# Optimization experiments

Hardware: AMD Instinct MI355X
Metric: run time of the kernel (lower is better)

Reference implementation:

```python
import jax, jax.numpy as jnp
import numpy as np

# Static config matching init_kwargs / forward constants
H = 12          # num_heads
D = 64          # head_dim
SW = 64         # kv_cache_sliding_window (frames)
SF = 8          # kv_cache_scale_frames
NUM_REG = 4     # num_register_tokens -> camera_idx=0, scale_idx=5
SPECIAL_END = NUM_REG + 2  # camera..scale inclusive slice = tokens [0:6)


def setup_inputs() -> dict:
    key = jax.random.key(0)
    ks = jax.random.split(key, 9)
    B, N, C = 1, 576, 768
    T = 192  # tokens per frame; num_frame_per_block = N // T = 3
    inp = {
        'x': jax.random.normal(ks[0], (B, N, C), jnp.float32),
        'qkv_w': jax.random.normal(ks[1], (3 * C, C), jnp.float32) * (C ** -0.5),
        'qkv_b': jax.random.normal(ks[2], (3 * C,), jnp.float32) * 0.02,
        'proj_w': jax.random.normal(ks[3], (C, C), jnp.float32) * (C ** -0.5),
        'proj_b': jax.random.normal(ks[4], (C,), jnp.float32) * 0.02,
        'k_cache': jax.random.normal(ks[5], (B, H, SW + SF, T, D), jnp.float32),
        'v_cache': jax.random.normal(ks[6], (B, H, SW + SF, T, D), jnp.float32),
        'k_special': jax.random.normal(ks[7], (B, H, 12, SPECIAL_END, D), jnp.float32),
        'v_special': jax.random.normal(ks[8], (B, H, 12, SPECIAL_END, D), jnp.float32),
    }
    return inp


def reference(x, qkv_w, qkv_b, proj_w, proj_b, k_cache, v_cache, k_special, v_special):
    B, N, C = x.shape
    T = k_cache.shape[3]           # tokens per frame
    nfb = N // T                   # num_frame_per_block (inferred, as in torch code)

    # qkv projection: (B,N,3C) -> (3,B,H,N,D)
    qkv = (x @ qkv_w.T + qkv_b).reshape(B, N, 3, H, D).transpose(2, 0, 3, 1, 4)
    q, k, v = qkv[0], qkv[1], qkv[2]   # each (B,H,N,D); q_norm/k_norm = Identity

    # Append new block frames to the cache
    k_cache = jnp.concatenate([k_cache, k.reshape(B, H, nfb, T, D)], axis=2)
    v_cache = jnp.concatenate([v_cache, v.reshape(B, H, nfb, T, D)], axis=2)

    # Sliding-window eviction (shapes chosen so this branch always fires)
    F = k_cache.shape[2]
    evict_start, evict_end = SF, F - SW   # 8 .. 11
    # cross-frame special tokens: camera..scale (tokens 0:6) of evicted frames
    new_sk = k_cache[:, :, evict_start:evict_end, :SPECIAL_END, :]
    new_sv = v_cache[:, :, evict_start:evict_end, :SPECIAL_END, :]
    k_special = jnp.concatenate([k_special, new_sk], axis=2)
    v_special = jnp.concatenate([v_special, new_sv], axis=2)
    # keep scale frames + last sliding_window frames
    k_cache = jnp.concatenate([k_cache[:, :, :SF], k_cache[:, :, -SW:]], axis=2)
    v_cache = jnp.concatenate([v_cache[:, :, :SF], v_cache[:, :, -SW:]], axis=2)

    # Flatten frames -> tokens; prepend special tokens
    k_full = jnp.concatenate([k_special.reshape(B, H, -1, D),
                              k_cache.reshape(B, H, -1, D)], axis=2)
    v_full = jnp.concatenate([v_special.reshape(B, H, -1, D),
                              v_cache.reshape(B, H, -1, D)], axis=2)

    # SDPA (no mask, no dropout, default scale 1/sqrt(D))
    scale = 1.0 / jnp.sqrt(jnp.float32(D))
    scores = jnp.einsum('bhnd,bhmd->bhnm', q, k_full) * scale
    attn = jax.nn.softmax(scores, axis=-1)
    out = jnp.einsum('bhnm,bhmd->bhnd', attn, v_full)

    out = out.transpose(0, 2, 1, 3).reshape(B, N, H * D)
    return out @ proj_w.T + proj_b
```

## Files before the change

### kernel.cpp

```cpp
#include <hip/hip_runtime.h>
#include <hip/hip_bf16.h>

#define NH    12
#define HD    64
#define NT    576
#define CC    768
#define M_TOT 13914
#define MP    13952
#define NTIL  218
#define NEW0  13338
#define SSTR  16

typedef short bf16x8 __attribute__((ext_vector_type(8)));
typedef float f32x4 __attribute__((ext_vector_type(4)));
typedef float f32x16 __attribute__((ext_vector_type(16)));

__device__ __forceinline__ unsigned pk2(float a, float b) {
  __hip_bfloat162 h = __float22bfloat162_rn(make_float2(a, b));
  return *(unsigned*)&h;
}

__global__ __launch_bounds__(256) void cvt_all(
    const float* __restrict__ x, const float* __restrict__ wsrc,
    __hip_bfloat16* __restrict__ xb, __hip_bfloat16* __restrict__ wb) {
  const int nx8 = NT * CC / 8;
  const int nw8 = 3 * CC * CC / 8;
  int i = blockIdx.x * 256 + threadIdx.x;
  const float* src;
  __hip_bfloat16* dst;
  int j;
  if (i < nx8) { src = x; dst = xb; j = i; }
  else { j = i - nx8; if (j >= nw8) return; src = wsrc; dst = wb; }
  const float4 a = ((const float4*)src)[2 * j];
  const float4 b = ((const float4*)src)[2 * j + 1];
  __hip_bfloat16 t[8];
  t[0] = __float2bfloat16(a.x); t[1] = __float2bfloat16(a.y);
  t[2] = __float2bfloat16(a.z); t[3] = __float2bfloat16(a.w);
  t[4] = __float2bfloat16(b.x); t[5] = __float2bfloat16(b.y);
  t[6] = __float2bfloat16(b.z); t[7] = __float2bfloat16(b.w);
  ((uint4*)dst)[j] = *(const uint4*)t;
}

__device__ __forceinline__ const float* kv_src_row(
    const float* __restrict__ cache, const float* __restrict__ special,
    int h, int m) {
  if (m < 72) return special + ((size_t)h * 72 + m) * HD;
  if (m < 90) {
    const int j = m - 72;
    return cache + (((size_t)h * 72 + 8 + j / 6) * 192 + (j % 6)) * HD;
  }
  if (m < 1626) return cache + ((size_t)h * 13824 + (m - 90)) * HD;
  return cache + ((size_t)h * 13824 + 2112 + (m - 1626)) * HD;
}

#define GEMM_BLKS 324
#define VT_BLKS   2616
#define KB_BLKS   10004

__global__ __launch_bounds__(256) void qkv_and_gather(
    const __hip_bfloat16* __restrict__ xb, const __hip_bfloat16* __restrict__ wb,
    const float* __restrict__ bias, __hip_bfloat16* __restrict__ Qb,
    __hip_bfloat16* __restrict__ Kf, __hip_bfloat16* __restrict__ Vt,
    const float* __restrict__ kc, const float* __restrict__ ksp,
    const float* __restrict__ vc, const float* __restrict__ vsp) {
  __shared__ float vsf[64][68];
  const int bx = blockIdx.x;
  const int tid = threadIdx.x;

  if (bx < GEMM_BLKS) {
    const int w = tid >> 6, l = tid & 63, l15 = l & 15, lg = l >> 4;
    const int n0 = (bx % 36) * 64;
    const int mw = (bx / 36) * 64 + w * 16;

    f32x4 acc[4];
#pragma unroll
    for (int nt = 0; nt < 4; ++nt) acc[nt] = (f32x4){0.f, 0.f, 0.f, 0.f};

    const __hip_bfloat16* arow = xb + (size_t)(mw + l15) * CC + 8 * lg;
#pragma unroll 4
    for (int k0 = 0; k0 < CC; k0 += 32) {
      const bf16x8 a = *(const bf16x8*)(arow + k0);
#pragma unroll
      for (int nt = 0; nt < 4; ++nt) {
        const bf16x8 b =
            *(const bf16x8*)(wb + (size_t)(n0 + nt * 16 + l15) * CC + k0 + 8 * lg);
        acc[nt] = __builtin_amdgcn_mfma_f32_16x16x32_bf16(a, b, acc[nt], 0, 0, 0);
      }
    }
#pragma unroll
    for (int nt = 0; nt < 4; ++nt) {
      const int c = n0 + nt * 16 + l15;
      const int which = c / CC;
      const int rem = c - which * CC;
      const int hh = rem >> 6;
      const int dd = rem & 63;
      const float bc = bias[c];
#pragma unroll
      for (int r = 0; r < 4; ++r) {
        const int m = mw + 4 * lg + r;
        const float v = acc[nt][r] + bc;
        if (which == 0) {
          Qb[((size_t)hh * NT + m) * HD + dd] = __float2bfloat16(v * 0.125f);
        } else if (which == 1) {
          Kf[((size_t)hh * MP + NEW0 + m) * HD + dd] = __float2bfloat16(v);
        } else {
          Vt[((size_t)hh * HD + dd) * MP + NEW0 + m] = __float2bfloat16(v);
        }
      }
    }
  } else if (bx < GEMM_BLKS + VT_BLKS) {
    const int tv = bx - GEMM_BLKS;
    const int m0 = (tv % 218) * 64;
    const int h = tv / 218;
    if (m0 >= NEW0) return;
#pragma unroll
    for (int p = 0; p < 4; ++p) {
      const int mr = m0 + p * 16 + (tid >> 4);
      const int c4 = (tid & 15) * 4;
      float4 v = make_float4(0.f, 0.f, 0.f, 0.f);
      if (mr < NEW0) v = *(const float4*)(kv_src_row(vc, vsp, h, mr) + c4);
      *(float4*)&vsf[p * 16 + (tid >> 4)][c4] = v;
    }
    __syncthreads();
#pragma unroll
    for (int e0 = 0; e0 < 2; ++e0) {
      const int e = tid + e0 * 256;
      const int d = e >> 3;
      const int ms = (e & 7) * 8;
      __hip_bfloat16 t[8];
#pragma unroll
      for (int j = 0; j < 8; ++j) t[j] = __float2bfloat16(vsf[ms + j][d]);
      __hip_bfloat16* dst = Vt + ((size_t)h * HD + d) * MP + m0 + ms;
      if (m0 + ms + 8 <= NEW0) {
        *(uint4*)dst = *(const uint4*)t;
      } else {
#pragma unroll
        for (int j = 0; j < 8; ++j)
          if (m0 + ms + j < NEW0) dst[j] = t[j];
      }
    }
  } else {
    const int idx = (bx - GEMM_BLKS - VT_BLKS) * 256 + tid;
    const int per_h = NEW0 * 16;
    if (idx >= NH * per_h) return;
    const int h = idx / per_h;
    const int r = idx - h * per_h;
    const int m = r >> 4;
    const int dq = (r & 15) << 2;
    const float4 v = *(const float4*)(kv_src_row(kc, ksp, h, m) + dq);
    __hip_bfloat162* dst = (__hip_bfloat162*)(Kf + ((size_t)h * MP + m) * HD + dq);
    __hip_bfloat162 a, b;
    a.x = __float2bfloat16(v.x); a.y = __float2bfloat16(v.y);
    b.x = __float2bfloat16(v.z); b.y = __float2bfloat16(v.w);
    dst[0] = a; dst[1] = b;
  }
}

__global__ __launch_bounds__(256, 4) void attn_partial(
    const __hip_bfloat16* __restrict__ Qb, const __hip_bfloat16* __restrict__ Kf,
    const __hip_bfloat16* __restrict__ Vt, float* __restrict__ Opart,
    float2* __restrict__ mlpart) {
  __shared__ __align__(16) char lds[16384];
  char* ksb = lds;
  char* vtb = lds + 8192;

  const int tid = threadIdx.x;
  const int w = tid >> 6, l = tid & 63;
  const int l31 = l & 31, hi = l >> 5;

  const int i = blockIdx.x;
  const int work = (i & 7) * 120 + (i >> 3);
  const int qt = work % 5;
  const int hs = work / 5;
  const int h = hs % NH;
  const int strip = hs / NH;

  const int qrow = qt * 128 + w * 32 + l31;
  const int qrc = qrow < NT ? qrow : NT - 1;

  bf16x8 qreg[4];
  {
    const __hip_bfloat16* qp = Qb + ((size_t)h * NT + qrc) * HD + 8 * hi;
#pragma unroll
    for (int s4 = 0; s4 < 4; ++s4) qreg[s4] = *(const bf16x8*)(qp + 16 * s4);
  }

  f32x16 oacc0, oacc1;
#pragma unroll
  for (int r = 0; r < 16; ++r) { oacc0[r] = 0.f; oacc1[r] = 0.f; }
  float m_run = -1e30f, l_run = 0.f;

  const __hip_bfloat16* Kh = Kf + (size_t)h * MP * HD;
  const __hip_bfloat16* Vth = Vt + (size_t)h * HD * MP;

  for (int t = strip; t < NTIL; t += SSTR) {
    const int m0 = t * 64;
#pragma unroll
    for (int e = 0; e < 2; ++e) {
      const int c = tid + 256 * e;
      const int row = c >> 3, p = c & 7;
      const unsigned off = ((unsigned)((row << 7) | (p << 4))) ^ ((row & 7) << 4);
      const uint4 kd = *(const uint4*)(Kh + (size_t)(m0 + row) * HD + p * 8);
      const uint4 vd = *(const uint4*)(Vth + (size_t)row * MP + m0 + p * 8);
      *(uint4*)(ksb + off) = kd;
      *(uint4*)(vtb + off) = vd;
    }
    __syncthreads();

    f32x16 sc0, sc1;
#pragma unroll
    for (int r = 0; r < 16; ++r) { sc0[r] = 0.f; sc1[r] = 0.f; }
#pragma unroll
    for (int s4 = 0; s4 < 4; ++s4) {
      const int cb = 32 * s4 + 16 * hi;
      const unsigned o0 = ((unsigned)((l31 << 7) | cb)) ^ ((l31 & 7) << 4);
      const unsigned o1 = ((unsigned)(((l31 + 32) << 7) | cb)) ^ ((l31 & 7) << 4);
      const bf16x8 a0 = *(const bf16x8*)(ksb + o0);
      const bf16x8 a1 = *(const bf16x8*)(ksb + o1);
      sc0 = __builtin_amdgcn_mfma_f32_32x32x16_bf16(a0, qreg[s4], sc0, 0, 0, 0);
      sc1 = __builtin_amdgcn_mfma_f32_32x32x16_bf16(a1, qreg[s4], sc1, 0, 0, 0);
    }

    if (m0 + 64 > M_TOT) {
#pragma unroll
      for (int r = 0; r < 16; ++r) {
        const int base = (r & 3) + 8 * (r >> 2) + 4 * hi;
        if (m0 + base >= M_TOT) sc0[r] = -1e30f;
        if (m0 + 32 + base >= M_TOT) sc1[r] = -1e30f;
      }
    }

    float mt = sc0[0];
#pragma unroll
    for (int r = 1; r < 16; ++r) mt = fmaxf(mt, sc0[r]);
#pragma unroll
    for (int r = 0; r < 16; ++r) mt = fmaxf(mt, sc1[r]);
    mt = fmaxf(mt, __shfl_xor(mt, 32));

    if (__any(mt > m_run + 8.f)) {
      const float mn = fmaxf(m_run, mt);
      const float corr = __expf(m_run - mn);
      m_run = mn;
      l_run *= corr;
#pragma unroll
      for (int r = 0; r < 16; ++r) { oacc0[r] *= corr; oacc1[r] *= corr; }
    }

    float psum = 0.f;
    unsigned W0[8], W1[8];
#pragma unroll
    for (int i2 = 0; i2 < 8; ++i2) {
      const float e0 = __expf(sc0[2 * i2] - m_run);
      const float e1 = __expf(sc0[2 * i2 + 1] - m_run);
      const float f0 = __expf(sc1[2 * i2] - m_run);
      const float f1 = __expf(sc1[2 * i2 + 1] - m_run);
      psum += (e0 + e1) + (f0 + f1);
      W0[i2] = pk2(e0, e1);
      W1[i2] = pk2(f0, f1);
    }
    psum += __shfl_xor(psum, 32);
    l_run += psum;

#pragma unroll
    for (int s4 = 0; s4 < 4; ++s4) {
      const int u = s4 & 1;
      const unsigned a0 = (s4 < 2) ? W0[4 * u + 0] : W1[4 * u + 0];
      const unsigned a1 = (s4 < 2) ? W0[4 * u + 1] : W1[4 * u + 1];
      const unsigned a2 = (s4 < 2) ? W0[4 * u + 2] : W1[4 * u + 2];
      const unsigned a3 = (s4 < 2) ? W0[4 * u + 3] : W1[4 * u + 3];
      const unsigned x0 = (unsigned)__shfl_xor((int)a0, 32);
      const unsigned x1 = (unsigned)__shfl_xor((int)a1, 32);
      const unsigned x2 = (unsigned)__shfl_xor((int)a2, 32);
      const unsigned x3 = (unsigned)__shfl_xor((int)a3, 32);
      union { unsigned u4[4]; bf16x8 v; } pa;
      pa.u4[0] = hi ? x2 : a0;
      pa.u4[1] = hi ? x3 : a1;
      pa.u4[2] = hi ? a2 : x0;
      pa.u4[3] = hi ? a3 : x1;
      const int cb = 32 * s4 + 16 * hi;
#pragma unroll
      for (int dh = 0; dh < 2; ++dh) {
        const int vr = 32 * dh + l31;
        const unsigned ov = ((unsigned)((vr << 7) | cb)) ^ ((vr & 7) << 4);
        const bf16x8 va = *(const bf16x8*)(vtb + ov);
        if (dh == 0)
          oacc0 = __builtin_amdgcn_mfma_f32_32x32x16_bf16(va, pa.v, oacc0, 0, 0, 0);
        else
          oacc1 = __builtin_amdgcn_mfma_f32_32x32x16_bf16(va, pa.v, oacc1, 0, 0, 0);
      }
    }
    __syncthreads();
  }

  if (qrow < NT) {
    float* Op = Opart + (((size_t)strip * NH + h) * NT + qrow) * HD;
#pragma unroll
    for (int g = 0; g < 4; ++g) {
      f32x4 o0 = {oacc0[4 * g], oacc0[4 * g + 1], oacc0[4 * g + 2], oacc0[4 * g + 3]};
      f32x4 o1 = {oacc1[4 * g], oacc1[4 * g + 1], oacc1[4 * g + 2], oacc1[4 * g + 3]};
      *(f32x4*)(Op + 8 * g + 4 * hi) = o0;
      *(f32x4*)(Op + 32 + 8 * g + 4 * hi) = o1;
    }
    if (hi == 0)
      mlpart[((size_t)strip * NH + h) * NT + qrow] = make_float2(m_run, l_run);
  }
}

__global__ __launch_bounds__(256) void attn_merge(
    const float* __restrict__ Opart, const float2* __restrict__ mlpart,
    float* __restrict__ Ow) {
  const int idx = blockIdx.x * 256 + threadIdx.x;
  if (idx >= NH * NT * HD) return;
  const int d = idx & 63;
  const int hn = idx >> 6;
  const int n = hn % NT;
  const int h = hn / NT;
  float M = -1e30f;
  float m[SSTR], lv[SSTR];
#pragma unroll
  for (int s = 0; s < SSTR; ++s) {
    const float2 ml = mlpart[((size_t)s * NH + h) * NT + n];
    m[s] = ml.x; lv[s] = ml.y;
    M = fmaxf(M, m[s]);
  }
  float L = 0.f, O = 0.f;
#pragma unroll
  for (int s = 0; s < SSTR; ++s) {
    const float e = __expf(m[s] - M);
    L += lv[s] * e;
    O += Opart[(((size_t)s * NH + h) * NT + n) * HD + d] * e;
  }
  Ow[(size_t)n * CC + h * HD + d] = O / L;
}

__global__ __launch_bounds__(256) void gemm_proj(
    const float* __restrict__ A, const float* __restrict__ W,
    const float* __restrict__ bias, float* __restrict__ out_f) {
  __shared__ float xs[32][36];
  __shared__ float wsT[32][68];
  const int tid = threadIdx.x;
  const int tx = tid & 15, ty = tid >> 4;
  const int bm = blockIdx.y * 32, bn = blockIdx.x * 64;
  float acc[2][4] = {{0.f, 0.f, 0.f, 0.f}, {0.f, 0.f, 0.f, 0.f}};
  for (int k0 = 0; k0 < CC; k0 += 32) {
    {
      const int r = tid >> 3, kq = (tid & 7) << 2;
      *(float4*)&xs[r][kq] = *(const float4*)(A + (size_t)(bm + r) * CC + k0 + kq);
    }
#pragma unroll
    for (int e0 = 0; e0 < 2; ++e0) {
      const int e = tid + e0 * 256;
      const int r = e >> 3, kq = (e & 7) << 2;
      float4 v = *(const float4*)(W + (size_t)(bn + r) * CC + k0 + kq);
      wsT[kq + 0][r] = v.x; wsT[kq + 1][r] = v.y;
      wsT[kq + 2][r] = v.z; wsT[kq + 3][r] = v.w;
    }
    __syncthreads();
#pragma unroll
    for (int kk = 0; kk < 32; ++kk) {
      const float a0 = xs[ty * 2 + 0][kk];
      const float a1 = xs[ty * 2 + 1][kk];
      const float4 b = *(const float4*)&wsT[kk][tx * 4];
      acc[0][0] = fmaf(a0, b.x, acc[0][0]); acc[0][1] = fmaf(a0, b.y, acc[0][1]);
      acc[0][2] = fmaf(a0, b.z, acc[0][2]); acc[0][3] = fmaf(a0, b.w, acc[0][3]);
      acc[1][0] = fmaf(a1, b.x, acc[1][0]); acc[1][1] = fmaf(a1, b.y, acc[1][1]);
      acc[1][2] = fmaf(a1, b.z, acc[1][2]); acc[1][3] = fmaf(a1, b.w, acc[1][3]);
    }
    __syncthreads();
  }
#pragma unroll
  for (int i = 0; i < 2; ++i)
#pragma unroll
    for (int j = 0; j < 4; ++j) {
      const int m = bm + ty * 2 + i, c = bn + tx * 4 + j;
      out_f[(size_t)m * CC + c] = acc[i][j] + bias[c];
    }
}

extern "C" void kernel_launch(void* const* d_in, const int* in_sizes, int n_in,
                              void* d_out, int out_size, void* d_ws,
                              size_t ws_size, hipStream_t stream) {
  const float* x       = (const float*)d_in[0];
  const float* qkv_w   = (const float*)d_in[1];
  const float* qkv_b   = (const float*)d_in[2];
  const float* proj_w  = (const float*)d_in[3];
  const float* proj_b  = (const float*)d_in[4];
  const float* k_cache = (const float*)d_in[5];
  const float* v_cache = (const float*)d_in[6];
  const float* k_specl = (const float*)d_in[7];
  const float* v_specl = (const float*)d_in[8];
  float* out = (float*)d_out;

  const size_t qb_bytes = (size_t)NH * NT * HD * 2;
  const size_t kv_bytes = (size_t)NH * MP * HD * 2;
  const size_t xb_bytes = (size_t)NT * CC * 2;
  const size_t op_bytes = (size_t)SSTR * NH * NT * HD * 4;
  const size_t ml_bytes = (size_t)SSTR * NH * NT * 8;

  char* ws = (char*)d_ws;
  __hip_bfloat16* Qb = (__hip_bfloat16*)ws;
  __hip_bfloat16* Kf = (__hip_bfloat16*)(ws + qb_bytes);
  __hip_bfloat16* Vt = (__hip_bfloat16*)(ws + qb_bytes + kv_bytes);
  char* opp = ws + qb_bytes + 2 * kv_bytes;
  float* Opart = (float*)opp;
  __hip_bfloat16* xb = (__hip_bfloat16*)opp;
  __hip_bfloat16* wb = (__hip_bfloat16*)(opp + xb_bytes);
  float2* mlpart = (float2*)(opp + op_bytes);
  float* Ow = (float*)(opp + op_bytes + ml_bytes);

  cvt_all<<<dim3(1080), 256, 0, stream>>>(x, qkv_w, xb, wb);
  qkv_and_gather<<<dim3(GEMM_BLKS + VT_BLKS + KB_BLKS), 256, 0, stream>>>(
      xb, wb, qkv_b, Qb, Kf, Vt, k_cache, k_specl, v_cache, v_specl);
  attn_partial<<<dim3(5 * NH * SSTR), 256, 0, stream>>>(Qb, Kf, Vt, Opart, mlpart);
  attn_merge<<<dim3((NH * NT * HD + 255) / 256), 256, 0, stream>>>(Opart, mlpart, Ow);
  gemm_proj<<<dim3(12, 18), 256, 0, stream>>>(Ow, proj_w, proj_b, out);
}
```

Measured before the change: 126.7 us.

## Double-buffer attention KV tiles, use exp2 softmax, MFMA split-bf16 output projection

The attention loop now prefetches the next K/V tile into registers and writes it to a second LDS buffer while computing on the current tile, so each tile needs one barrier instead of separate load/sync phases. The softmax switches to exp2 by folding log2(e) into the Q scale. The fp32 FMA output projection is replaced by an MFMA GEMM that uses hi/lo bf16 splits of the activations and weights, keeping accuracy near fp32. The strip count is chosen from workspace size, and Kf space is reused for the bf16 output. This adds proj-weight conversion work and doubles LDS use per block, which may lower occupancy.

```diff
diff --git a/kernel.cpp b/kernel.cpp
--- a/kernel.cpp
+++ b/kernel.cpp
@@ -9,12 +9,13 @@
 #define MP    13952
 #define NTIL  218
 #define NEW0  13338
-#define SSTR  16
 
 typedef short bf16x8 __attribute__((ext_vector_type(8)));
 typedef float f32x4 __attribute__((ext_vector_type(4)));
 typedef float f32x16 __attribute__((ext_vector_type(16)));
 
+#define QSCALE 0.18033688011112042f
+
 __device__ __forceinline__ unsigned pk2(float a, float b) {
   __hip_bfloat162 h = __float22bfloat162_rn(make_float2(a, b));
   return *(unsigned*)&h;
@@ -22,23 +23,42 @@
 
 __global__ __launch_bounds__(256) void cvt_all(
     const float* __restrict__ x, const float* __restrict__ wsrc,
-    __hip_bfloat16* __restrict__ xb, __hip_bfloat16* __restrict__ wb) {
+    const float* __restrict__ pw, __hip_bfloat16* __restrict__ xb,
+    __hip_bfloat16* __restrict__ wb, __hip_bfloat16* __restrict__ wph,
+    __hip_bfloat16* __restrict__ wpl) {
   const int nx8 = NT * CC / 8;
   const int nw8 = 3 * CC * CC / 8;
+  const int npw8 = CC * CC / 8;
   int i = blockIdx.x * 256 + threadIdx.x;
-  const float* src;
-  __hip_bfloat16* dst;
-  int j;
-  if (i < nx8) { src = x; dst = xb; j = i; }
-  else { j = i - nx8; if (j >= nw8) return; src = wsrc; dst = wb; }
-  const float4 a = ((const float4*)src)[2 * j];
-  const float4 b = ((const float4*)src)[2 * j + 1];
-  __hip_bfloat16 t[8];
-  t[0] = __float2bfloat16(a.x); t[1] = __float2bfloat16(a.y);
-  t[2] = __float2bfloat16(a.z); t[3] = __float2bfloat16(a.w);
-  t[4] = __float2bfloat16(b.x); t[5] = __float2bfloat16(b.y);
-  t[6] = __float2bfloat16(b.z); t[7] = __float2bfloat16(b.w);
-  ((uint4*)dst)[j] = *(const uint4*)t;
+  if (i < nx8 + nw8) {
+    const float* src; __hip_bfloat16* dst; int j;
+    if (i < nx8) { src = x; dst = xb; j = i; }
+    else { j = i - nx8; src = wsrc; dst = wb; }
+    const float4 a = ((const float4*)src)[2 * j];
+    const float4 b = ((const float4*)src)[2 * j + 1];
+    __hip_bfloat16 t[8];
+    t[0] = __float2bfloat16(a.x); t[1] = __float2bfloat16(a.y);
+    t[2] = __float2bfloat16(a.z); t[3] = __float2bfloat16(a.w);
+    t[4] = __float2bfloat16(b.x); t[5] = __float2bfloat16(b.y);
+    t[6] = __float2bfloat16(b.z); t[7] = __float2bfloat16(b.w);
+    ((uint4*)dst)[j] = *(const uint4*)t;
+  } else {
+    const int j = i - nx8 - nw8;
+    if (j >= npw8) return;
+    float v[8];
+    const float4 a = ((const float4*)pw)[2 * j];
+    const float4 b = ((const float4*)pw)[2 * j + 1];
+    v[0] = a.x; v[1] = a.y; v[2] = a.z; v[3] = a.w;
+    v[4] = b.x; v[5] = b.y; v[6] = b.z; v[7] = b.w;
+    __hip_bfloat16 th[8], tl[8];
+#pragma unroll
+    for (int e = 0; e < 8; ++e) {
+      th[e] = __float2bfloat16(v[e]);
+      tl[e] = __float2bfloat16(v[e] - __bfloat162float(th[e]));
+    }
+    ((uint4*)wph)[j] = *(const uint4*)th;
+    ((uint4*)wpl)[j] = *(const uint4*)tl;
+  }
 }
 
 __device__ __forceinline__ const float* kv_src_row(
@@ -100,7 +120,7 @@
         const int m = mw + 4 * lg + r;
         const float v = acc[nt][r] + bc;
         if (which == 0) {
-          Qb[((size_t)hh * NT + m) * HD + dd] = __float2bfloat16(v * 0.125f);
+          Qb[((size_t)hh * NT + m) * HD + dd] = __float2bfloat16(v * QSCALE);
         } else if (which == 1) {
           Kf[((size_t)hh * MP + NEW0 + m) * HD + dd] = __float2bfloat16(v);
         } else {
@@ -156,20 +176,20 @@
   }
 }
 
+template <int S>
 __global__ __launch_bounds__(256, 4) void attn_partial(
     const __hip_bfloat16* __restrict__ Qb, const __hip_bfloat16* __restrict__ Kf,
     const __hip_bfloat16* __restrict__ Vt, float* __restrict__ Opart,
     float2* __restrict__ mlpart) {
-  __shared__ __align__(16) char lds[16384];
-  char* ksb = lds;
-  char* vtb = lds + 8192;
+  __shared__ __align__(16) char lds[32768];
 
   const int tid = threadIdx.x;
   const int w = tid >> 6, l = tid & 63;
   const int l31 = l & 31, hi = l >> 5;
 
   const int i = blockIdx.x;
-  const int work = (i & 7) * 120 + (i >> 3);
+  const int per_xcd = (5 * NH * S) / 8;
+  const int work = (i & 7) * per_xcd + (i >> 3);
   const int qt = work % 5;
   const int hs = work / 5;
   const int h = hs % NH;
@@ -193,19 +213,41 @@
   const __hip_bfloat16* Kh = Kf + (size_t)h * MP * HD;
   const __hip_bfloat16* Vth = Vt + (size_t)h * HD * MP;
 
-  for (int t = strip; t < NTIL; t += SSTR) {
+  const int srow0 = tid >> 3;
+  const int srow1 = 32 + (tid >> 3);
+  const int sp8 = (tid & 7) * 8;
+  const unsigned soff0 =
+      ((unsigned)((srow0 << 7) | ((tid & 7) << 4))) ^ ((srow0 & 7) << 4);
+  const unsigned soff1 =
+      ((unsigned)((srow1 << 7) | ((tid & 7) << 4))) ^ ((srow1 & 7) << 4);
+
+  uint4 kd0, kd1, vd0, vd1;
+  auto issue = [&](int t) {
     const int m0 = t * 64;
-#pragma unroll
-    for (int e = 0; e < 2; ++e) {
-      const int c = tid + 256 * e;
-      const int row = c >> 3, p = c & 7;
-      const unsigned off = ((unsigned)((row << 7) | (p << 4))) ^ ((row & 7) << 4);
-      const uint4 kd = *(const uint4*)(Kh + (size_t)(m0 + row) * HD + p * 8);
-      const uint4 vd = *(const uint4*)(Vth + (size_t)row * MP + m0 + p * 8);
-      *(uint4*)(ksb + off) = kd;
-      *(uint4*)(vtb + off) = vd;
-    }
-    __syncthreads();
+    kd0 = *(const uint4*)(Kh + (size_t)(m0 + srow0) * HD + sp8);
+    kd1 = *(const uint4*)(Kh + (size_t)(m0 + srow1) * HD + sp8);
+    vd0 = *(const uint4*)(Vth + (size_t)srow0 * MP + m0 + sp8);
+    vd1 = *(const uint4*)(Vth + (size_t)srow1 * MP + m0 + sp8);
+  };
+  auto commit = [&](char* buf) {
+    *(uint4*)(buf + soff0) = kd0;
+    *(uint4*)(buf + soff1) = kd1;
+    *(uint4*)(buf + 8192 + soff0) = vd0;
+    *(uint4*)(buf + 8192 + soff1) = vd1;
+  };
+
+  issue(strip);
+  commit(lds);
+  __syncthreads();
+
+  int cur = 0;
+  for (int t = strip; t < NTIL; t += S) {
+    const int tn = t + S;
+    if (tn < NTIL) issue(tn);
+
+    char* ksb = lds + (cur << 14);
+    char* vtb = ksb + 8192;
+    const int m0 = t * 64;
 
     f32x16 sc0, sc1;
 #pragma unroll
@@ -239,7 +281,7 @@
 
     if (__any(mt > m_run + 8.f)) {
       const float mn = fmaxf(m_run, mt);
-      const float corr = __expf(m_run - mn);
+      const float corr = exp2f(m_run - mn);
       m_run = mn;
       l_run *= corr;
 #pragma unroll
@@ -250,10 +292,10 @@
     unsigned W0[8], W1[8];
 #pragma unroll
     for (int i2 = 0; i2 < 8; ++i2) {
-      const float e0 = __expf(sc0[2 * i2] - m_run);
-      const float e1 = __expf(sc0[2 * i2 + 1] - m_run);
-      const float f0 = __expf(sc1[2 * i2] - m_run);
-      const float f1 = __expf(sc1[2 * i2 + 1] - m_run);
+      const float e0 = exp2f(sc0[2 * i2] - m_run);
+      const float e1 = exp2f(sc0[2 * i2 + 1] - m_run);
+      const float f0 = exp2f(sc1[2 * i2] - m_run);
+      const float f1 = exp2f(sc1[2 * i2 + 1] - m_run);
       psum += (e0 + e1) + (f0 + f1);
       W0[i2] = pk2(e0, e1);
       W1[i2] = pk2(f0, f1);
@@ -289,7 +331,10 @@
           oacc1 = __builtin_amdgcn_mfma_f32_32x32x16_bf16(va, pa.v, oacc1, 0, 0, 0);
       }
     }
+
+    if (tn < NTIL) commit(lds + ((cur ^ 1) << 14));
     __syncthreads();
+    cur ^= 1;
   }
 
   if (qrow < NT) {
@@ -306,9 +351,10 @@
   }
 }
 
+template <int S>
 __global__ __launch_bounds__(256) void attn_merge(
     const float* __restrict__ Opart, const float2* __restrict__ mlpart,
-    float* __restrict__ Ow) {
+    __hip_bfloat16* __restrict__ Owh, __hip_bfloat16* __restrict__ Owl) {
   const int idx = blockIdx.x * 256 + threadIdx.x;
   if (idx >= NH * NT * HD) return;
   const int d = idx & 63;
@@ -316,65 +362,64 @@
   const int n = hn % NT;
   const int h = hn / NT;
   float M = -1e30f;
-  float m[SSTR], lv[SSTR];
-#pragma unroll
-  for (int s = 0; s < SSTR; ++s) {
+  float m[S], lv[S];
+#pragma unroll
+  for (int s = 0; s < S; ++s) {
     const float2 ml = mlpart[((size_t)s * NH + h) * NT + n];
     m[s] = ml.x; lv[s] = ml.y;
     M = fmaxf(M, m[s]);
   }
   float L = 0.f, O = 0.f;
 #pragma unroll
-  for (int s = 0; s < SSTR; ++s) {
-    const float e = __expf(m[s] - M);
+  for (int s = 0; s < S; ++s) {
+    const float e = exp2f(m[s] - M);
     L += lv[s] * e;
     O += Opart[(((size_t)s * NH + h) * NT + n) * HD + d] * e;
   }
-  Ow[(size_t)n * CC + h * HD + d] = O / L;
-}
-
-__global__ __launch_bounds__(256) void gemm_proj(
-    const float* __restrict__ A, const float* __restrict__ W,
+  const float v = O / L;
+  const __hip_bfloat16 hB = __float2bfloat16(v);
+  const size_t o = (size_t)n * CC + h * HD + d;
+  Owh[o] = hB;
+  Owl[o] = __float2bfloat16(v - __bfloat162float(hB));
+}
+
+__global__ __launch_bounds__(256) void gemm_proj_mfma(
+    const __hip_bfloat16* __restrict__ Ah, const __hip_bfloat16* __restrict__ Al,
+    const __hip_bfloat16* __restrict__ Wh, const __hip_bfloat16* __restrict__ Wl,
     const float* __restrict__ bias, float* __restrict__ out_f) {
-  __shared__ float xs[32][36];
-  __shared__ float wsT[32][68];
   const int tid = threadIdx.x;
-  const int tx = tid & 15, ty = tid >> 4;
-  const int bm = blockIdx.y * 32, bn = blockIdx.x * 64;
-  float acc[2][4] = {{0.f, 0.f, 0.f, 0.f}, {0.f, 0.f, 0.f, 0.f}};
+  const int w = tid >> 6, l = tid & 63, l15 = l & 15, lg = l >> 4;
+  const int n0 = blockIdx.x * 64;
+  const int mw = blockIdx.y * 64 + w * 16;
+
+  f32x4 acc[4];
+#pragma unroll
+  for (int nt = 0; nt < 4; ++nt) acc[nt] = (f32x4){0.f, 0.f, 0.f, 0.f};
+
+  const __hip_bfloat16* ah = Ah + (size_t)(mw + l15) * CC + 8 * lg;
+  const __hip_bfloat16* al = Al + (size_t)(mw + l15) * CC + 8 * lg;
+#pragma unroll 2
   for (int k0 = 0; k0 < CC; k0 += 32) {
-    {
-      const int r = tid >> 3, kq = (tid & 7) << 2;
-      *(float4*)&xs[r][kq] = *(const float4*)(A + (size_t)(bm + r) * CC + k0 + kq);
-    }
-#pragma unroll
-    for (int e0 = 0; e0 < 2; ++e0) {
-      const int e = tid + e0 * 256;
-      const int r = e >> 3, kq = (e & 7) << 2;
-      float4 v = *(const float4*)(W + (size_t)(bn + r) * CC + k0 + kq);
-      wsT[kq + 0][r] = v.x; wsT[kq + 1][r] = v.y;
-      wsT[kq + 2][r] = v.z; wsT[kq + 3][r] = v.w;
-    }
-    __syncthreads();
-#pragma unroll
-    for (int kk = 0; kk < 32; ++kk) {
-      const float a0 = xs[ty * 2 + 0][kk];
-      const float a1 = xs[ty * 2 + 1][kk];
-      const float4 b = *(const float4*)&wsT[kk][tx * 4];
-      acc[0][0] = fmaf(a0, b.x, acc[0][0]); acc[0][1] = fmaf(a0, b.y, acc[0][1]);
-      acc[0][2] = fmaf(a0, b.z, acc[0][2]); acc[0][3] = fmaf(a0, b.w, acc[0][3]);
-      acc[1][0] = fmaf(a1, b.x, acc[1][0]); acc[1][1] = fmaf(a1, b.y, acc[1][1]);
-      acc[1][2] = fmaf(a1, b.z, acc[1][2]); acc[1][3] = fmaf(a1, b.w, acc[1][3]);
-    }
-    __syncthreads();
-  }
-#pragma unroll
-  for (int i = 0; i < 2; ++i)
-#pragma unroll
-    for (int j = 0; j < 4; ++j) {
-      const int m = bm + ty * 2 + i, c = bn + tx * 4 + j;
-      out_f[(size_t)m * CC + c] = acc[i][j] + bias[c];
-    }
+    const bf16x8 a0 = *(const bf16x8*)(ah + k0);
+    const bf16x8 a1 = *(const bf16x8*)(al + k0);
+#pragma unroll
+    for (int nt = 0; nt < 4; ++nt) {
+      const size_t wi = (size_t)(n0 + nt * 16 + l15) * CC + k0 + 8 * lg;
+      const bf16x8 bh = *(const bf16x8*)(Wh + wi);
+      const bf16x8 bl = *(const bf16x8*)(Wl + wi);
+      acc[nt] = __builtin_amdgcn_mfma_f32_16x16x32_bf16(a0, bh, acc[nt], 0, 0, 0);
+      acc[nt] = __builtin_amdgcn_mfma_f32_16x16x32_bf16(a0, bl, acc[nt], 0, 0, 0);
+      acc[nt] = __builtin_amdgcn_mfma_f32_16x16x32_bf16(a1, bh, acc[nt], 0, 0, 0);
+    }
+  }
+#pragma unroll
+  for (int nt = 0; nt < 4; ++nt) {
+    const int c = n0 + nt * 16 + l15;
+    const float bc = bias[c];
+#pragma unroll
+    for (int r = 0; r < 4; ++r)
+      out_f[(size_t)(mw + 4 * lg + r) * CC + c] = acc[nt][r] + bc;
+  }
 }
 
 extern "C" void kernel_launch(void* const* d_in, const int* in_sizes, int n_in,
@@ -394,24 +439,47 @@
   const size_t qb_bytes = (size_t)NH * NT * HD * 2;
   const size_t kv_bytes = (size_t)NH * MP * HD * 2;
   const size_t xb_bytes = (size_t)NT * CC * 2;
-  const size_t op_bytes = (size_t)SSTR * NH * NT * HD * 4;
-  const size_t ml_bytes = (size_t)SSTR * NH * NT * 8;
+  const size_t wb_bytes = (size_t)3 * CC * CC * 2;
+  const size_t pw_bytes = (size_t)CC * CC * 2;
+  const size_t owh_bytes = (size_t)NT * CC * 2;
+
+  auto need = [&](int S) -> size_t {
+    const size_t op = (size_t)S * NH * NT * HD * 4;
+    const size_t ml = (size_t)S * NH * NT * 8;
+    const size_t opr = op > xb_bytes + wb_bytes ? op : xb_bytes + wb_bytes;
+    return qb_bytes + 2 * kv_bytes + opr + ml + 2 * pw_bytes;
+  };
+  const int S = (need(16) <= ws_size) ? 16 : 8;
+  const size_t op_bytes = (size_t)S * NH * NT * HD * 4;
+  const size_t ml_bytes = (size_t)S * NH * NT * 8;
+  const size_t opr = op_bytes > xb_bytes + wb_bytes ? op_bytes : xb_bytes + wb_bytes;
 
   char* ws = (char*)d_ws;
   __hip_bfloat16* Qb = (__hip_bfloat16*)ws;
-  __hip_bfloat16* Kf = (__hip_bfloat16*)(ws + qb_bytes);
-  __hip_bfloat16* Vt = (__hip_bfloat16*)(ws + qb_bytes + kv_bytes);
-  char* opp = ws + qb_bytes + 2 * kv_bytes;
+  char* kf_region = ws + qb_bytes;
+  __hip_bfloat16* Kf = (__hip_bfloat16*)kf_region;
+  __hip_bfloat16* Vt = (__hip_bfloat16*)(kf_region + kv_bytes);
+  char* opp = kf_region + 2 * kv_bytes;
   float* Opart = (float*)opp;
   __hip_bfloat16* xb = (__hip_bfloat16*)opp;
   __hip_bfloat16* wb = (__hip_bfloat16*)(opp + xb_bytes);
-  float2* mlpart = (float2*)(opp + op_bytes);
-  float* Ow = (float*)(opp + op_bytes + ml_bytes);
-
-  cvt_all<<<dim3(1080), 256, 0, stream>>>(x, qkv_w, xb, wb);
+  float2* mlpart = (float2*)(opp + opr);
+  __hip_bfloat16* wph = (__hip_bfloat16*)(opp + opr + ml_bytes);
+  __hip_bfloat16* wpl = (__hip_bfloat16*)(opp + opr + ml_bytes + pw_bytes);
+  __hip_bfloat16* Owh = (__hip_bfloat16*)kf_region;
+  __hip_bfloat16* Owl = (__hip_bfloat16*)(kf_region + owh_bytes);
+
+  cvt_all<<<dim3(1368), 256, 0, stream>>>(x, qkv_w, proj_w, xb, wb, wph, wpl);
   qkv_and_gather<<<dim3(GEMM_BLKS + VT_BLKS + KB_BLKS), 256, 0, stream>>>(
       xb, wb, qkv_b, Qb, Kf, Vt, k_cache, k_specl, v_cache, v_specl);
-  attn_partial<<<dim3(5 * NH * SSTR), 256, 0, stream>>>(Qb, Kf, Vt, Opart, mlpart);
-  attn_merge<<<dim3((NH * NT * HD + 255) / 256), 256, 0, stream>>>(Opart, mlpart, Ow);
-  gemm_proj<<<dim3(12, 18), 256, 0, stream>>>(Ow, proj_w, proj_b, out);
-}
+  if (S == 16) {
+    attn_partial<16><<<dim3(5 * NH * 16), 256, 0, stream>>>(Qb, Kf, Vt, Opart, mlpart);
+    attn_merge<16><<<dim3((NH * NT * HD + 255) / 256), 256, 0, stream>>>(
+        Opart, mlpart, Owh, Owl);
+  } else {
+    attn_partial<8><<<dim3(5 * NH * 8), 256, 0, stream>>>(Qb, Kf, Vt, Opart, mlpart);
+    attn_merge<8><<<dim3((NH * NT * HD + 255) / 256), 256, 0, stream>>>(
+        Opart, mlpart, Owh, Owl);
+  }
+  gemm_proj_mfma<<<dim3(12, 9), 256, 0, stream>>>(Owh, Owl, wph, wpl, proj_b, out);
+}
```

Measured after the change: 141.4 us. 1.12x slower.
